# Optimization experiments

Measured on AMD Instinct MI355X. Metric: run time of the kernel, lower is better.

## Reference

```python
import jax, jax.numpy as jnp
import numpy as np
import math

B, S, H = 2, 2048, 1024
NH, HD = 16, 64
MAX_SCALE = 4


def setup_inputs() -> dict:
    key = jax.random.key(0)
    ks = jax.random.split(key, 8)
    s = 0.02
    return {
        "x": jax.random.normal(ks[0], (B, S, H), dtype=jnp.float32),
        "Wqkv": jax.random.normal(ks[1], (H, 3 * H), dtype=jnp.float32) * s,
        "bqkv": jnp.zeros((3 * H,), dtype=jnp.float32),
        "Wout": jax.random.normal(ks[2], (H, H), dtype=jnp.float32) * s,
        "bout": jnp.zeros((H,), dtype=jnp.float32),
        "Wscale": jax.random.normal(ks[3], (H, MAX_SCALE), dtype=jnp.float32) * s,
        "bscale": jnp.zeros((MAX_SCALE,), dtype=jnp.float32),
    }


def reference(x, Wqkv, bqkv, Wout, bout, Wscale, bscale):
    b, s, h = x.shape
    inv_sqrt_hd = 1.0 / math.sqrt(HD)
    # qkv projection -> [3, b, nh, s, hd]
    qkv = (x @ Wqkv + bqkv).reshape(b, s, 3, NH, HD).transpose(2, 0, 3, 1, 4)
    q, k, v = qkv[0], qkv[1], qkv[2]
    # per-token soft weights over scales [b, s, max_scale]
    scale_weights = jax.nn.softmax(x @ Wscale + bscale, axis=-1)
    out = jnp.zeros((b, NH, s, HD), dtype=x.dtype)
    for scale_idx in range(MAX_SCALE):
        dilation = 2 ** scale_idx
        kd = k[:, :, ::dilation]  # strided (dilated) gather of keys
        vd = v[:, :, ::dilation]
        scores = jnp.einsum("bhqd,bhkd->bhqk", q, kd) * inv_sqrt_hd
        attn = jax.nn.softmax(scores, axis=-1)
        o = jnp.einsum("bhqk,bhkd->bhqd", attn, vd)
        w = scale_weights[:, :, scale_idx][:, None, :, None]  # [b,1,s,1]
        out = out + o * w
    out = out.transpose(0, 2, 1, 3).reshape(b, s, h)
    return out @ Wout + bout
```

## Files before the change

### kernel.cpp

```cpp
#include <hip/hip_runtime.h>
#include <stdint.h>

typedef unsigned short u16;
typedef __attribute__((ext_vector_type(8))) __bf16 bf8v;
typedef __attribute__((ext_vector_type(4))) float f4v;
typedef __attribute__((ext_vector_type(16))) float f16v;

#define BB 2
#define SS 2048
#define HH 1024

#define OFF_Q   0u
#define OFF_K0  8388608u
#define OFF_K1  16777216u
#define OFF_K2  20971520u
#define OFF_K3  23068672u
#define OFF_V0  24117248u
#define OFF_V1  32505856u
#define OFF_V2  36700160u
#define OFF_V3  38797312u
#define OFF_WQT 39845888u
#define OFF_WOT 46137344u
#define OFF_XB  48234496u
#define OFF_SCW 56623104u
#define OFF_P1  56688640u
#define WS_SPLIT_NEED 65077248u

__device__ __forceinline__ u16 f2bf(float f) {
    union { float f; uint32_t u; } v; v.f = f;
    uint32_t r = v.u + 0x7fffu + ((v.u >> 16) & 1u);
    return (u16)(r >> 16);
}
__device__ __forceinline__ uint32_t pk2(float a, float b) {
    return (uint32_t)f2bf(a) | ((uint32_t)f2bf(b) << 16);
}
__device__ __forceinline__ uint32_t pkt2(float a, float b) {
    union { float f; uint32_t u; } x, y; x.f = a; y.f = b;
    return (x.u >> 16) | (y.u & 0xffff0000u);
}
__device__ __forceinline__ uint32_t addbf2(uint32_t a, uint32_t b) {
    float a0 = __uint_as_float(a << 16), a1 = __uint_as_float(a & 0xffff0000u);
    float b0 = __uint_as_float(b << 16), b1 = __uint_as_float(b & 0xffff0000u);
    return pk2(a0 + b0, a1 + b1);
}

__global__ __launch_bounds__(256) void xconv_kernel(const float* __restrict__ x,
                                                    u16* __restrict__ xb) {
    size_t t = (size_t)blockIdx.x * 256 + threadIdx.x;
    float4 v = *(const float4*)&x[t * 4];
    uint2 pk; pk.x = pk2(v.x, v.y); pk.y = pk2(v.z, v.w);
    *(uint2*)&xb[t * 4] = pk;
}

__global__ __launch_bounds__(256) void wconv_kernel(const float* __restrict__ W,
                                                    u16* __restrict__ Wt,
                                                    int N, int K) {
    __shared__ float tile[64][69];
    const int tid = threadIdx.x;
    const int n0 = blockIdx.x * 64, k0 = blockIdx.y * 64;
    const int r = tid >> 4, c4 = (tid & 15) * 4;
#pragma unroll
    for (int it = 0; it < 4; it++) {
        float4 v = *(const float4*)&W[(size_t)(k0 + it * 16 + r) * N + n0 + c4];
        tile[it * 16 + r][c4 + 0] = v.x; tile[it * 16 + r][c4 + 1] = v.y;
        tile[it * 16 + r][c4 + 2] = v.z; tile[it * 16 + r][c4 + 3] = v.w;
    }
    __syncthreads();
#pragma unroll
    for (int it = 0; it < 4; it++) {
        int n = it * 16 + r;
        uint2 pk;
        pk.x = pk2(tile[c4 + 0][n], tile[c4 + 1][n]);
        pk.y = pk2(tile[c4 + 2][n], tile[c4 + 3][n]);
        *(uint2*)&Wt[(size_t)(n0 + n) * K + k0 + c4] = pk;
    }
}

__global__ __launch_bounds__(256) void scale_kernel(const float* __restrict__ x,
                                                    const float* __restrict__ Wscale,
                                                    const float* __restrict__ bscale,
                                                    float* __restrict__ scw) {
    const int lane = threadIdx.x & 63;
    const int wid  = threadIdx.x >> 6;
    const int row  = blockIdx.x * 4 + wid;
    float a0 = 0.f, a1 = 0.f, a2 = 0.f, a3 = 0.f;
    for (int i = 0; i < 16; i++) {
        int hh = lane + i * 64;
        float xs = x[(size_t)row * HH + hh];
        float4 wv = *(const float4*)&Wscale[hh * 4];
        a0 += xs * wv.x; a1 += xs * wv.y; a2 += xs * wv.z; a3 += xs * wv.w;
    }
    for (int off = 1; off < 64; off <<= 1) {
        a0 += __shfl_xor(a0, off); a1 += __shfl_xor(a1, off);
        a2 += __shfl_xor(a2, off); a3 += __shfl_xor(a3, off);
    }
    if (lane == 0) {
        a0 += bscale[0]; a1 += bscale[1]; a2 += bscale[2]; a3 += bscale[3];
        float mx = fmaxf(fmaxf(a0, a1), fmaxf(a2, a3));
        float e0 = __expf(a0 - mx), e1 = __expf(a1 - mx);
        float e2 = __expf(a2 - mx), e3 = __expf(a3 - mx);
        float inv = 1.f / (e0 + e1 + e2 + e3);
        float4 o = {e0 * inv, e1 * inv, e2 * inv, e3 * inv};
        *(float4*)&scw[(size_t)row * 4] = o;
    }
}

template<int MODE>
__global__ __launch_bounds__(256) void gemm_bt(const u16* __restrict__ A,
                                               const u16* __restrict__ A2,
                                               const u16* __restrict__ Bt,
                                               const float* __restrict__ bias,
                                               void* __restrict__ Cp,
                                               int N, int K) {
    __shared__ __align__(16) u16 At[128 * 40];
    __shared__ __align__(16) u16 Btl[128 * 40];
    const int tid  = threadIdx.x;
    const int lane = tid & 63;
    const int wid  = tid >> 6;
    const int l15  = lane & 15;
    const int quad = lane >> 4;
    const int wm = wid & 1, wn = wid >> 1;
    const int m0 = blockIdx.y * 128;
    const int n0 = blockIdx.x * 128;
    const int srow = tid >> 2;
    const int sc8  = (tid & 3) * 8;

    f4v acc[4][4];
#pragma unroll
    for (int i = 0; i < 4; i++)
#pragma unroll
        for (int j = 0; j < 4; j++) acc[i][j] = (f4v){0.f, 0.f, 0.f, 0.f};

    uint4 pa0 = *(const uint4*)(A  + (size_t)(m0 + srow) * K + sc8);
    uint4 pa1 = *(const uint4*)(A  + (size_t)(m0 + srow + 64) * K + sc8);
    uint4 pb0 = *(const uint4*)(Bt + (size_t)(n0 + srow) * K + sc8);
    uint4 pb1 = *(const uint4*)(Bt + (size_t)(n0 + srow + 64) * K + sc8);
    uint4 qa0, qa1;
    if (MODE == 2) {
        qa0 = *(const uint4*)(A2 + (size_t)(m0 + srow) * K + sc8);
        qa1 = *(const uint4*)(A2 + (size_t)(m0 + srow + 64) * K + sc8);
    }

    for (int kc = 0; kc < K; kc += 32) {
        __syncthreads();
        if (MODE == 2) {
            uint4 w0, w1;
            w0.x = addbf2(pa0.x, qa0.x); w0.y = addbf2(pa0.y, qa0.y);
            w0.z = addbf2(pa0.z, qa0.z); w0.w = addbf2(pa0.w, qa0.w);
            w1.x = addbf2(pa1.x, qa1.x); w1.y = addbf2(pa1.y, qa1.y);
            w1.z = addbf2(pa1.z, qa1.z); w1.w = addbf2(pa1.w, qa1.w);
            *(uint4*)&At[srow * 40 + sc8]        = w0;
            *(uint4*)&At[(srow + 64) * 40 + sc8] = w1;
        } else {
            *(uint4*)&At[srow * 40 + sc8]        = pa0;
            *(uint4*)&At[(srow + 64) * 40 + sc8] = pa1;
        }
        *(uint4*)&Btl[srow * 40 + sc8]        = pb0;
        *(uint4*)&Btl[(srow + 64) * 40 + sc8] = pb1;
        __syncthreads();
        if (kc + 32 < K) {
            pa0 = *(const uint4*)(A  + (size_t)(m0 + srow) * K + kc + 32 + sc8);
            pa1 = *(const uint4*)(A  + (size_t)(m0 + srow + 64) * K + kc + 32 + sc8);
            pb0 = *(const uint4*)(Bt + (size_t)(n0 + srow) * K + kc + 32 + sc8);
            pb1 = *(const uint4*)(Bt + (size_t)(n0 + srow + 64) * K + kc + 32 + sc8);
            if (MODE == 2) {
                qa0 = *(const uint4*)(A2 + (size_t)(m0 + srow) * K + kc + 32 + sc8);
                qa1 = *(const uint4*)(A2 + (size_t)(m0 + srow + 64) * K + kc + 32 + sc8);
            }
        }
        bf8v af[4], bf[4];
#pragma unroll
        for (int t = 0; t < 4; t++) {
            af[t] = *(const bf8v*)&At[(wm * 64 + t * 16 + l15) * 40 + quad * 8];
            bf[t] = *(const bf8v*)&Btl[(wn * 64 + t * 16 + l15) * 40 + quad * 8];
        }
#pragma unroll
        for (int ti = 0; ti < 4; ti++)
#pragma unroll
            for (int tj = 0; tj < 4; tj++)
                acc[ti][tj] = __builtin_amdgcn_mfma_f32_16x16x32_bf16(af[ti], bf[tj], acc[ti][tj], 0, 0, 0);
    }

    if (MODE != 1) {
#pragma unroll
        for (int ti = 0; ti < 4; ti++)
#pragma unroll
            for (int tj = 0; tj < 4; tj++)
#pragma unroll
                for (int r = 0; r < 4; r++) {
                    int m = m0 + wm * 64 + ti * 16 + quad * 4 + r;
                    int n = n0 + wn * 64 + tj * 16 + l15;
                    ((float*)Cp)[(size_t)m * N + n] = acc[ti][tj][r] + bias[n];
                }
    } else {
        char* ws = (char*)Cp;
        u16* Qd = (u16*)ws;
        u16* K0 = (u16*)(ws + OFF_K0); u16* K1 = (u16*)(ws + OFF_K1);
        u16* K2 = (u16*)(ws + OFF_K2); u16* K3 = (u16*)(ws + OFF_K3);
        u16* V0 = (u16*)(ws + OFF_V0); u16* V1 = (u16*)(ws + OFF_V1);
        u16* V2 = (u16*)(ws + OFF_V2); u16* V3 = (u16*)(ws + OFF_V3);
        const int region = n0 >> 10;
        if (region == 0) {
#pragma unroll
            for (int ti = 0; ti < 4; ti++)
#pragma unroll
                for (int tj = 0; tj < 4; tj++)
#pragma unroll
                    for (int r = 0; r < 4; r++) {
                        int m = m0 + wm * 64 + ti * 16 + quad * 4 + r;
                        int n = n0 + wn * 64 + tj * 16 + l15;
                        Qd[(size_t)m * 1024 + n] = f2bf(acc[ti][tj][r] + bias[n]);
                    }
        } else if (region == 1) {
#pragma unroll
            for (int ti = 0; ti < 4; ti++)
#pragma unroll
                for (int tj = 0; tj < 4; tj++) {
                    int n  = n0 + wn * 64 + tj * 16 + l15;
                    int nk = n - 1024;
                    int h = nk >> 6, hd = nk & 63;
#pragma unroll
                    for (int r = 0; r < 4; r++) {
                        int m = m0 + wm * 64 + ti * 16 + quad * 4 + r;
                        int bb = m >> 11, tok = m & 2047;
                        int bh = bb * 16 + h;
                        u16 bv = f2bf((acc[ti][tj][r] + bias[n]) * 0.125f);
                        K0[((size_t)bh * 2048 + tok) * 64 + hd] = bv;
                        if (!(r & 1)) K1[((size_t)bh * 1024 + (tok >> 1)) * 64 + hd] = bv;
                        if (r == 0) {
                            K2[((size_t)bh * 512 + (tok >> 2)) * 64 + hd] = bv;
                            if (!(quad & 1)) K3[((size_t)bh * 256 + (tok >> 3)) * 64 + hd] = bv;
                        }
                    }
                }
        } else {
#pragma unroll
            for (int ti = 0; ti < 4; ti++)
#pragma unroll
                for (int tj = 0; tj < 4; tj++) {
                    int n  = n0 + wn * 64 + tj * 16 + l15;
                    int nv = n - 2048;
                    int h = nv >> 6, hd = nv & 63;
                    int tokb = m0 + wm * 64 + ti * 16 + quad * 4;
                    int bb = tokb >> 11, tok = tokb & 2047;
                    int bh = bb * 16 + h;
                    float v0 = acc[ti][tj][0] + bias[n];
                    float v1 = acc[ti][tj][1] + bias[n];
                    float v2 = acc[ti][tj][2] + bias[n];
                    float v3 = acc[ti][tj][3] + bias[n];
                    u16 c0 = f2bf(v0), c1 = f2bf(v1), c2 = f2bf(v2), c3 = f2bf(v3);
                    uint2 pk;
                    pk.x = (uint32_t)c0 | ((uint32_t)c1 << 16);
                    pk.y = (uint32_t)c2 | ((uint32_t)c3 << 16);
                    *(uint2*)&V0[((size_t)bh * 64 + hd) * 2048 + tok] = pk;
                    *(uint32_t*)&V1[((size_t)bh * 64 + hd) * 1024 + (tok >> 1)] =
                        (uint32_t)c0 | ((uint32_t)c2 << 16);
                    V2[((size_t)bh * 64 + hd) * 512 + (tok >> 2)] = c0;
                    if (!(quad & 1)) V3[((size_t)bh * 64 + hd) * 256 + (tok >> 3)] = c0;
                }
        }
    }
}

__global__ void attn_kernel(const char* __restrict__ ws, int split) {
    __shared__ __align__(16) u16 smem[14848];
    u16* Kt0 = smem;
    u16* Kt1 = smem + 2304;
    u16* Vt0 = smem + 4608;
    u16* Vt1 = smem + 7168;
    u16* Pt  = smem + 9728;

    const u16* Qd    = (const u16*)(ws + OFF_Q);
    const float* scw = (const float*)(ws + OFF_SCW);

    int b, s_lo, s_hi;
    u16* outp;
    if (split) {
        b = blockIdx.z >> 1;
        if ((blockIdx.z & 1) == 0) { s_lo = 0; s_hi = 0; outp = (u16*)(ws + OFF_XB); }
        else                       { s_lo = 1; s_hi = 3; outp = (u16*)(ws + OFF_P1); }
    } else {
        b = blockIdx.z; s_lo = 0; s_hi = 3;
        outp = (u16*)(ws + OFF_Q);
    }

    const int tid  = threadIdx.x;
    const int lane = tid & 63;
    const int wid  = tid >> 6;
    const int l31  = lane & 31;
    const int half = lane >> 5;
    const int h = blockIdx.y;
    const int q  = blockIdx.x * 128 + wid * 32 + l31;
    const int bh = b * 16 + h;

    const int skey = tid >> 3;
    const int shd8 = (tid & 7) * 8;
    const int svhd = tid >> 2;
    const int svk8 = (tid & 3) * 8;

    bf8v qf[4];
#pragma unroll
    for (int ks = 0; ks < 4; ks++)
        qf[ks] = *(const bf8v*)(Qd + (size_t)(b * SS + q) * 1024 + h * 64 + ks * 16 + half * 8);

    u16* Pw = Pt + wid * 1280;

    f16v ofin[2];
#pragma unroll
    for (int ht = 0; ht < 2; ht++)
#pragma unroll
        for (int r = 0; r < 16; r++) ofin[ht][r] = 0.f;

    const uint32_t koff[4] = {OFF_K0, OFF_K1, OFF_K2, OFF_K3};
    const uint32_t voff[4] = {OFF_V0, OFF_V1, OFF_V2, OFF_V3};

    for (int s = s_lo; s <= s_hi; s++) {
        const int Ss = SS >> s;
        const int nch = Ss >> 5;
        const u16* Kb = (const u16*)(ws + koff[s]) + (size_t)bh * Ss * 64;
        const u16* Vb = (const u16*)(ws + voff[s]) + (size_t)bh * 64 * Ss;

        f16v oacc[2];
#pragma unroll
        for (int ht = 0; ht < 2; ht++)
#pragma unroll
            for (int r = 0; r < 16; r++) oacc[ht][r] = 0.f;
        float ls = 0.f;

        uint4 kr = *(const uint4*)(Kb + (size_t)skey * 64 + shd8);
        uint4 vr = *(const uint4*)(Vb + (size_t)svhd * Ss + svk8);
        *(uint4*)&Kt0[skey * 72 + shd8] = kr;
        *(uint4*)&Vt0[svhd * 40 + svk8] = vr;
        if (nch > 1) {
            kr = *(const uint4*)(Kb + (size_t)(32 + skey) * 64 + shd8);
            vr = *(const uint4*)(Vb + (size_t)svhd * Ss + 32 + svk8);
        }
        __syncthreads();

        for (int c = 0; c < nch; c++) {
            u16* Ktc = (c & 1) ? Kt1 : Kt0;
            u16* Vtc = (c & 1) ? Vt1 : Vt0;
            u16* Ktn = (c & 1) ? Kt0 : Kt1;
            u16* Vtn = (c & 1) ? Vt0 : Vt1;
            f16v sa;
#pragma unroll
            for (int r = 0; r < 16; r++) sa[r] = 0.f;
#pragma unroll
            for (int ks = 0; ks < 4; ks++) {
                bf8v ka = *(const bf8v*)&Ktc[l31 * 72 + ks * 16 + half * 8];
                sa = __builtin_amdgcn_mfma_f32_32x32x16_bf16(ka, qf[ks], sa, 0, 0, 0);
            }
#pragma unroll
            for (int g = 0; g < 4; g++) {
                float e0 = __expf(sa[g * 4 + 0]);
                float e1 = __expf(sa[g * 4 + 1]);
                float e2 = __expf(sa[g * 4 + 2]);
                float e3 = __expf(sa[g * 4 + 3]);
                ls += (e0 + e1) + (e2 + e3);
                uint2 pk;
                pk.x = pkt2(e0, e1);
                pk.y = pkt2(e2, e3);
                *(uint2*)&Pw[l31 * 40 + g * 8 + half * 4] = pk;
            }
            if (c + 1 < nch) {
                *(uint4*)&Ktn[skey * 72 + shd8] = kr;
                *(uint4*)&Vtn[svhd * 40 + svk8] = vr;
            }
            if (c + 2 < nch) {
                kr = *(const uint4*)(Kb + (size_t)((c + 2) * 32 + skey) * 64 + shd8);
                vr = *(const uint4*)(Vb + (size_t)svhd * Ss + (c + 2) * 32 + svk8);
            }
            __asm__ volatile("s_waitcnt lgkmcnt(0)" ::: "memory");
#pragma unroll
            for (int kst = 0; kst < 2; kst++) {
                bf8v pb = *(const bf8v*)&Pw[l31 * 40 + kst * 16 + half * 8];
#pragma unroll
                for (int ht = 0; ht < 2; ht++) {
                    bf8v va = *(const bf8v*)&Vtc[(ht * 32 + l31) * 40 + kst * 16 + half * 8];
                    oacc[ht] = __builtin_amdgcn_mfma_f32_32x32x16_bf16(va, pb, oacc[ht], 0, 0, 0);
                }
            }
            __syncthreads();
        }
        ls += __shfl_xor(ls, 32);
        float w = scw[(size_t)(b * SS + q) * 4 + s] / ls;
#pragma unroll
        for (int ht = 0; ht < 2; ht++)
#pragma unroll
            for (int r = 0; r < 16; r++) ofin[ht][r] += w * oacc[ht][r];
    }
    const size_t base = (size_t)(b * SS + q) * 1024 + h * 64;
#pragma unroll
    for (int ht = 0; ht < 2; ht++)
#pragma unroll
        for (int g = 0; g < 4; g++) {
            uint2 pk;
            pk.x = pk2(ofin[ht][g * 4 + 0], ofin[ht][g * 4 + 1]);
            pk.y = pk2(ofin[ht][g * 4 + 2], ofin[ht][g * 4 + 3]);
            *(uint2*)&outp[base + ht * 32 + g * 8 + half * 4] = pk;
        }
}

extern "C" void kernel_launch(void* const* d_in, const int* in_sizes, int n_in,
                              void* d_out, int out_size, void* d_ws, size_t ws_size,
                              hipStream_t stream) {
    const float* x      = (const float*)d_in[0];
    const float* Wqkv   = (const float*)d_in[1];
    const float* bqkv   = (const float*)d_in[2];
    const float* Wout   = (const float*)d_in[3];
    const float* bout   = (const float*)d_in[4];
    const float* Wscale = (const float*)d_in[5];
    const float* bscale = (const float*)d_in[6];
    float* out = (float*)d_out;

    char* ws = (char*)d_ws;
    u16*   wqt   = (u16*)(ws + OFF_WQT);
    u16*   wot   = (u16*)(ws + OFF_WOT);
    u16*   xb    = (u16*)(ws + OFF_XB);
    float* scw   = (float*)(ws + OFF_SCW);
    const int split = (ws_size >= (size_t)WS_SPLIT_NEED) ? 1 : 0;

    xconv_kernel<<<dim3(4096), dim3(256), 0, stream>>>(x, xb);
    wconv_kernel<<<dim3(48, 16), dim3(256), 0, stream>>>(Wqkv, wqt, 3072, 1024);
    wconv_kernel<<<dim3(16, 16), dim3(256), 0, stream>>>(Wout, wot, 1024, 1024);
    scale_kernel<<<dim3(1024), dim3(256), 0, stream>>>(x, Wscale, bscale, scw);
    gemm_bt<1><<<dim3(24, 32), dim3(256), 0, stream>>>(
        xb, nullptr, wqt, bqkv, (void*)ws, 3072, 1024);
    attn_kernel<<<dim3(16, 16, split ? 4 : 2), dim3(256), 0, stream>>>(ws, split);
    if (split) {
        gemm_bt<2><<<dim3(8, 32), dim3(256), 0, stream>>>(
            (const u16*)(ws + OFF_XB), (const u16*)(ws + OFF_P1), wot, bout,
            (void*)out, 1024, 1024);
    } else {
        gemm_bt<0><<<dim3(8, 32), dim3(256), 0, stream>>>(
            (const u16*)(ws + OFF_Q), nullptr, wot, bout, (void*)out, 1024, 1024);
    }
}
```

Before: 280.6 us.

## Keep softmax probabilities in registers and fold x conversion into scale kernel

The attention kernel now shuffles the exponentiated probabilities across wave halves to build the MFMA B operand directly in registers. This removes the per-wave LDS staging buffer and its lgkmcnt wait, and shrinks shared memory. The x-to-bf16 conversion is merged into the scale kernel, which removes one launch and one read of x. The split-path partial-sum addition moves out of the output GEMM's inner loop into a separate combine kernel, which adds a launch and an extra pass over memory.

```diff
diff --git a/kernel.cpp b/kernel.cpp
--- a/kernel.cpp
+++ b/kernel.cpp
@@ -44,12 +44,14 @@
     return pk2(a0 + b0, a1 + b1);
 }
 
-__global__ __launch_bounds__(256) void xconv_kernel(const float* __restrict__ x,
-                                                    u16* __restrict__ xb) {
+__global__ __launch_bounds__(256) void combine_kernel(const u16* __restrict__ p0,
+                                                      const u16* __restrict__ p1,
+                                                      u16* __restrict__ pc) {
     size_t t = (size_t)blockIdx.x * 256 + threadIdx.x;
-    float4 v = *(const float4*)&x[t * 4];
-    uint2 pk; pk.x = pk2(v.x, v.y); pk.y = pk2(v.z, v.w);
-    *(uint2*)&xb[t * 4] = pk;
+    uint2 a = *(const uint2*)&p0[t * 4];
+    uint2 b = *(const uint2*)&p1[t * 4];
+    uint2 o; o.x = addbf2(a.x, b.x); o.y = addbf2(a.y, b.y);
+    *(uint2*)&pc[t * 4] = o;
 }
 
 __global__ __launch_bounds__(256) void wconv_kernel(const float* __restrict__ W,
@@ -79,7 +81,8 @@
 __global__ __launch_bounds__(256) void scale_kernel(const float* __restrict__ x,
                                                     const float* __restrict__ Wscale,
                                                     const float* __restrict__ bscale,
-                                                    float* __restrict__ scw) {
+                                                    float* __restrict__ scw,
+                                                    u16* __restrict__ xb) {
     const int lane = threadIdx.x & 63;
     const int wid  = threadIdx.x >> 6;
     const int row  = blockIdx.x * 4 + wid;
@@ -87,6 +90,7 @@
     for (int i = 0; i < 16; i++) {
         int hh = lane + i * 64;
         float xs = x[(size_t)row * HH + hh];
+        xb[(size_t)row * HH + hh] = f2bf(xs);
         float4 wv = *(const float4*)&Wscale[hh * 4];
         a0 += xs * wv.x; a1 += xs * wv.y; a2 += xs * wv.z; a3 += xs * wv.w;
     }
@@ -107,7 +111,6 @@
 
 template<int MODE>
 __global__ __launch_bounds__(256) void gemm_bt(const u16* __restrict__ A,
-                                               const u16* __restrict__ A2,
                                                const u16* __restrict__ Bt,
                                                const float* __restrict__ bias,
                                                void* __restrict__ Cp,
@@ -135,26 +138,11 @@
     uint4 pa1 = *(const uint4*)(A  + (size_t)(m0 + srow + 64) * K + sc8);
     uint4 pb0 = *(const uint4*)(Bt + (size_t)(n0 + srow) * K + sc8);
     uint4 pb1 = *(const uint4*)(Bt + (size_t)(n0 + srow + 64) * K + sc8);
-    uint4 qa0, qa1;
-    if (MODE == 2) {
-        qa0 = *(const uint4*)(A2 + (size_t)(m0 + srow) * K + sc8);
-        qa1 = *(const uint4*)(A2 + (size_t)(m0 + srow + 64) * K + sc8);
-    }
 
     for (int kc = 0; kc < K; kc += 32) {
         __syncthreads();
-        if (MODE == 2) {
-            uint4 w0, w1;
-            w0.x = addbf2(pa0.x, qa0.x); w0.y = addbf2(pa0.y, qa0.y);
-            w0.z = addbf2(pa0.z, qa0.z); w0.w = addbf2(pa0.w, qa0.w);
-            w1.x = addbf2(pa1.x, qa1.x); w1.y = addbf2(pa1.y, qa1.y);
-            w1.z = addbf2(pa1.z, qa1.z); w1.w = addbf2(pa1.w, qa1.w);
-            *(uint4*)&At[srow * 40 + sc8]        = w0;
-            *(uint4*)&At[(srow + 64) * 40 + sc8] = w1;
-        } else {
-            *(uint4*)&At[srow * 40 + sc8]        = pa0;
-            *(uint4*)&At[(srow + 64) * 40 + sc8] = pa1;
-        }
+        *(uint4*)&At[srow * 40 + sc8]         = pa0;
+        *(uint4*)&At[(srow + 64) * 40 + sc8]  = pa1;
         *(uint4*)&Btl[srow * 40 + sc8]        = pb0;
         *(uint4*)&Btl[(srow + 64) * 40 + sc8] = pb1;
         __syncthreads();
@@ -163,10 +151,6 @@
             pa1 = *(const uint4*)(A  + (size_t)(m0 + srow + 64) * K + kc + 32 + sc8);
             pb0 = *(const uint4*)(Bt + (size_t)(n0 + srow) * K + kc + 32 + sc8);
             pb1 = *(const uint4*)(Bt + (size_t)(n0 + srow + 64) * K + kc + 32 + sc8);
-            if (MODE == 2) {
-                qa0 = *(const uint4*)(A2 + (size_t)(m0 + srow) * K + kc + 32 + sc8);
-                qa1 = *(const uint4*)(A2 + (size_t)(m0 + srow + 64) * K + kc + 32 + sc8);
-            }
         }
         bf8v af[4], bf[4];
 #pragma unroll
@@ -181,7 +165,7 @@
                 acc[ti][tj] = __builtin_amdgcn_mfma_f32_16x16x32_bf16(af[ti], bf[tj], acc[ti][tj], 0, 0, 0);
     }
 
-    if (MODE != 1) {
+    if (MODE == 0) {
 #pragma unroll
         for (int ti = 0; ti < 4; ti++)
 #pragma unroll
@@ -263,12 +247,11 @@
 }
 
 __global__ void attn_kernel(const char* __restrict__ ws, int split) {
-    __shared__ __align__(16) u16 smem[14848];
+    __shared__ __align__(16) u16 smem[9728];
     u16* Kt0 = smem;
     u16* Kt1 = smem + 2304;
     u16* Vt0 = smem + 4608;
     u16* Vt1 = smem + 7168;
-    u16* Pt  = smem + 9728;
 
     const u16* Qd    = (const u16*)(ws + OFF_Q);
     const float* scw = (const float*)(ws + OFF_SCW);
@@ -303,8 +286,6 @@
     for (int ks = 0; ks < 4; ks++)
         qf[ks] = *(const bf8v*)(Qd + (size_t)(b * SS + q) * 1024 + h * 64 + ks * 16 + half * 8);
 
-    u16* Pw = Pt + wid * 1280;
-
     f16v ofin[2];
 #pragma unroll
     for (int ht = 0; ht < 2; ht++)
@@ -350,6 +331,7 @@
                 bf8v ka = *(const bf8v*)&Ktc[l31 * 72 + ks * 16 + half * 8];
                 sa = __builtin_amdgcn_mfma_f32_32x32x16_bf16(ka, qf[ks], sa, 0, 0, 0);
             }
+            uint2 tg[4];
 #pragma unroll
             for (int g = 0; g < 4; g++) {
                 float e0 = __expf(sa[g * 4 + 0]);
@@ -357,11 +339,24 @@
                 float e2 = __expf(sa[g * 4 + 2]);
                 float e3 = __expf(sa[g * 4 + 3]);
                 ls += (e0 + e1) + (e2 + e3);
-                uint2 pk;
-                pk.x = pkt2(e0, e1);
-                pk.y = pkt2(e2, e3);
-                *(uint2*)&Pw[l31 * 40 + g * 8 + half * 4] = pk;
-            }
+                tg[g].x = pkt2(e0, e1);
+                tg[g].y = pkt2(e2, e3);
+            }
+            uint2 sg[4];
+#pragma unroll
+            for (int g = 0; g < 4; g++) {
+                sg[g].x = __shfl_xor(tg[g].x, 32);
+                sg[g].y = __shfl_xor(tg[g].y, 32);
+            }
+            uint4 pbu[2];
+            pbu[0].x = half ? sg[1].x : tg[0].x;
+            pbu[0].y = half ? sg[1].y : tg[0].y;
+            pbu[0].z = half ? tg[1].x : sg[0].x;
+            pbu[0].w = half ? tg[1].y : sg[0].y;
+            pbu[1].x = half ? sg[3].x : tg[2].x;
+            pbu[1].y = half ? sg[3].y : tg[2].y;
+            pbu[1].z = half ? tg[3].x : sg[2].x;
+            pbu[1].w = half ? tg[3].y : sg[2].y;
             if (c + 1 < nch) {
                 *(uint4*)&Ktn[skey * 72 + shd8] = kr;
                 *(uint4*)&Vtn[svhd * 40 + svk8] = vr;
@@ -370,10 +365,9 @@
                 kr = *(const uint4*)(Kb + (size_t)((c + 2) * 32 + skey) * 64 + shd8);
                 vr = *(const uint4*)(Vb + (size_t)svhd * Ss + (c + 2) * 32 + svk8);
             }
-            __asm__ volatile("s_waitcnt lgkmcnt(0)" ::: "memory");
 #pragma unroll
             for (int kst = 0; kst < 2; kst++) {
-                bf8v pb = *(const bf8v*)&Pw[l31 * 40 + kst * 16 + half * 8];
+                bf8v pb = *(const bf8v*)&pbu[kst];
 #pragma unroll
                 for (int ht = 0; ht < 2; ht++) {
                     bf8v va = *(const bf8v*)&Vtc[(ht * 32 + l31) * 40 + kst * 16 + half * 8];
@@ -420,19 +414,15 @@
     float* scw   = (float*)(ws + OFF_SCW);
     const int split = (ws_size >= (size_t)WS_SPLIT_NEED) ? 1 : 0;
 
-    xconv_kernel<<<dim3(4096), dim3(256), 0, stream>>>(x, xb);
     wconv_kernel<<<dim3(48, 16), dim3(256), 0, stream>>>(Wqkv, wqt, 3072, 1024);
     wconv_kernel<<<dim3(16, 16), dim3(256), 0, stream>>>(Wout, wot, 1024, 1024);
-    scale_kernel<<<dim3(1024), dim3(256), 0, stream>>>(x, Wscale, bscale, scw);
-    gemm_bt<1><<<dim3(24, 32), dim3(256), 0, stream>>>(
-        xb, nullptr, wqt, bqkv, (void*)ws, 3072, 1024);
+    scale_kernel<<<dim3(1024), dim3(256), 0, stream>>>(x, Wscale, bscale, scw, xb);
+    gemm_bt<1><<<dim3(24, 32), dim3(256), 0, stream>>>(xb, wqt, bqkv, (void*)ws, 3072, 1024);
     attn_kernel<<<dim3(16, 16, split ? 4 : 2), dim3(256), 0, stream>>>(ws, split);
     if (split) {
-        gemm_bt<2><<<dim3(8, 32), dim3(256), 0, stream>>>(
-            (const u16*)(ws + OFF_XB), (const u16*)(ws + OFF_P1), wot, bout,
-            (void*)out, 1024, 1024);
-    } else {
-        gemm_bt<0><<<dim3(8, 32), dim3(256), 0, stream>>>(
-            (const u16*)(ws + OFF_Q), nullptr, wot, bout, (void*)out, 1024, 1024);
-    }
-}
+        combine_kernel<<<dim3(4096), dim3(256), 0, stream>>>(
+            (const u16*)(ws + OFF_XB), (const u16*)(ws + OFF_P1), (u16*)(ws + OFF_Q));
+    }
+    gemm_bt<0><<<dim3(8, 32), dim3(256), 0, stream>>>(
+        (const u16*)(ws + OFF_Q), wot, bout, (void*)out, 1024, 1024);
+}
```

New measurement: 276.6 us. Within noise of the previous version (-1.5%).
